# Optimization experiments

Measured on AMD Instinct MI355X. Metric: run time of the kernel, lower is better.

Reference implementation:

```python
import jax, jax.numpy as jnp
import numpy as np

B, S, HID = 2, 1024, 4096
N_HEADS, N_KV_HEADS = 32, 8
HEAD_DIM = HID // N_HEADS          # 128
N_REP = N_HEADS // N_KV_HEADS      # 4
ROPE_THETA = 10000.0


def setup_inputs() -> dict:
    key = jax.random.key(0)
    ks = jax.random.split(key, 5)
    scale = 0.02  # keep logits in a sane range
    return {
        "hidden_states": jax.random.normal(ks[0], (B, S, HID), dtype=jnp.float32),
        "Wq": jax.random.normal(ks[1], (HID, HID), dtype=jnp.float32) * scale,
        "Wk": jax.random.normal(ks[2], (N_KV_HEADS * HEAD_DIM, HID), dtype=jnp.float32) * scale,
        "Wv": jax.random.normal(ks[3], (N_KV_HEADS * HEAD_DIM, HID), dtype=jnp.float32) * scale,
        "Wo": jax.random.normal(ks[4], (HID, HID), dtype=jnp.float32) * scale,
    }


def _rope(x, cos, sin):
    # x: [B, H, S, D]; pairs are adjacent (view_as_complex on reshape(..., -1, 2))
    xe = x[..., 0::2]
    xo = x[..., 1::2]
    # cos/sin: [S, D/2] -> broadcast [1, 1, S, D/2]
    oe = xe * cos - xo * sin
    oo = xe * sin + xo * cos
    return jnp.stack([oe, oo], axis=-1).reshape(x.shape)


def reference(hidden_states, Wq, Wk, Wv, Wo):
    b, s, _ = hidden_states.shape
    q = (hidden_states @ Wq.T).reshape(b, s, N_HEADS, HEAD_DIM).transpose(0, 2, 1, 3)
    k = (hidden_states @ Wk.T).reshape(b, s, N_KV_HEADS, HEAD_DIM).transpose(0, 2, 1, 3)
    v = (hidden_states @ Wv.T).reshape(b, s, N_KV_HEADS, HEAD_DIM).transpose(0, 2, 1, 3)

    # RoPE (prefill: positions = arange(s))
    pos = jnp.arange(s, dtype=jnp.float32)
    inv_freq = 1.0 / (ROPE_THETA ** (jnp.arange(0, HEAD_DIM, 2, dtype=jnp.float32) / HEAD_DIM))
    freqs = pos[:, None] * inv_freq[None, :]  # [S, D/2]
    cos, sin = jnp.cos(freqs), jnp.sin(freqs)
    q = _rope(q, cos, sin)
    k = _rope(k, cos, sin)

    # GQA: repeat kv heads (repeat_kv expands each kv head n_rep times contiguously)
    k = jnp.repeat(k, N_REP, axis=1)  # [B, nH, S, D]
    v = jnp.repeat(v, N_REP, axis=1)

    scores = jnp.einsum("bhsd,bhtd->bhst", q, k) / jnp.sqrt(jnp.float32(HEAD_DIM))
    causal = jnp.tril(jnp.ones((s, s), dtype=bool))  # [S, S]
    scores = jnp.where(causal[None, None], scores, jnp.finfo(scores.dtype).min)
    attn = jax.nn.softmax(scores, axis=-1)
    out = jnp.einsum("bhst,bhtd->bhsd", attn, v)  # [B, nH, S, D]
    out = out.transpose(0, 2, 1, 3).reshape(b, s, HID)
    return out @ Wo.T
```

## Files before the change

kernel.cpp:

```cpp
#include <hip/hip_runtime.h>

typedef unsigned int u32;
typedef unsigned short u16;

#define S_LEN 1024
#define NH 32
#define NKV 8
#define DW 64
#define NEG_BIG (-1e30f)

typedef __bf16 bf16x8 __attribute__((ext_vector_type(8)));
typedef float f32x4 __attribute__((ext_vector_type(4)));

__device__ __forceinline__ u16 f2bf(float f) {
  u32 u = __builtin_bit_cast(u32, f);
  u += 0x7fffu + ((u >> 16) & 1u);
  return (u16)(u >> 16);
}
__device__ __forceinline__ float bflo(u32 u) { return __builtin_bit_cast(float, u << 16); }
__device__ __forceinline__ float bfhi(u32 u) { return __builtin_bit_cast(float, u & 0xffff0000u); }

__device__ __forceinline__ void gl_lds16(const u16* g, u32* l) {
  __builtin_amdgcn_global_load_lds(
      (__attribute__((address_space(1))) void*)const_cast<u16*>(g),
      (__attribute__((address_space(3))) void*)l, 16, 0, 0);
}

__launch_bounds__(256)
__global__ void cvt_bf16(const float4* __restrict__ in, uint4* __restrict__ out, int n8) {
  int i = blockIdx.x * 256 + threadIdx.x;
  if (i >= n8) return;
  float4 a = in[2 * i], b = in[2 * i + 1];
  uint4 o;
  o.x = (u32)f2bf(a.x) | ((u32)f2bf(a.y) << 16);
  o.y = (u32)f2bf(a.z) | ((u32)f2bf(a.w) << 16);
  o.z = (u32)f2bf(b.x) | ((u32)f2bf(b.y) << 16);
  o.w = (u32)f2bf(b.z) | ((u32)f2bf(b.w) << 16);
  out[i] = o;
}

template <bool BF16OUT, bool SPLIT>
__launch_bounds__(256)
__global__ void gemm16(const u16* __restrict__ A, const u16* __restrict__ B,
                       void* __restrict__ Cv, void* __restrict__ Cv2,
                       int M, int N, int K) {
  __shared__ u32 As[128 * 16];
  __shared__ u32 Bs[128 * 16];
  const int tid = threadIdx.x;
  const int lane = tid & 63, w = tid >> 6;
  const int wr = w >> 1, wc = w & 1;
  const int col = lane & 15, quad = lane >> 4;
  const int nwg = gridDim.x * gridDim.y;
  const int bid = blockIdx.y * gridDim.x + blockIdx.x;
  const int cpx = nwg >> 3;
  const int sw = (bid & 7) * cpx + (bid >> 3);
  const int m0 = (sw / gridDim.x) * 128, n0 = (sw % gridDim.x) * 128;

  const u16* ap0 = A + (size_t)(m0 + (tid >> 2)) * K + (tid & 3) * 8;
  const u16* ap1 = ap0 + (size_t)64 * K;
  const u16* bp0 = B + (size_t)(n0 + (tid >> 2)) * K + (tid & 3) * 8;
  const u16* bp1 = bp0 + (size_t)64 * K;
  u32* asd0 = &As[w * 256];
  u32* asd1 = &As[1024 + w * 256];
  u32* bsd0 = &Bs[w * 256];
  u32* bsd1 = &Bs[1024 + w * 256];

  f32x4 acc[4][4] = {};

  for (int k0 = 0; k0 < K; k0 += 32) {
    gl_lds16(ap0 + k0, asd0);
    gl_lds16(ap1 + k0, asd1);
    gl_lds16(bp0 + k0, bsd0);
    gl_lds16(bp1 + k0, bsd1);
    __syncthreads();

    bf16x8 af[4], bfr[4];
#pragma unroll
    for (int i = 0; i < 4; ++i) {
      int m = wr * 64 + i * 16 + col;
      af[i] = *reinterpret_cast<const bf16x8*>(&As[m * 16 + quad * 4]);
      int n = wc * 64 + i * 16 + col;
      bfr[i] = *reinterpret_cast<const bf16x8*>(&Bs[n * 16 + quad * 4]);
    }
#pragma unroll
    for (int i = 0; i < 4; ++i)
#pragma unroll
      for (int j = 0; j < 4; ++j)
        acc[i][j] = __builtin_amdgcn_mfma_f32_16x16x32_bf16(af[i], bfr[j], acc[i][j], 0, 0, 0);
    __syncthreads();
  }

#pragma unroll
  for (int i = 0; i < 4; ++i)
#pragma unroll
    for (int j = 0; j < 4; ++j)
#pragma unroll
      for (int r = 0; r < 4; ++r) {
        int row = m0 + wr * 64 + i * 16 + quad * 4 + r;
        int cc  = n0 + wc * 64 + j * 16 + col;
        float v = acc[i][j][r];
        if constexpr (SPLIT) {
          u16* dst = (cc >> 10) ? (u16*)Cv2 : (u16*)Cv;
          dst[(size_t)row * 1024 + (cc & 1023)] = f2bf(v);
        } else if constexpr (BF16OUT) {
          ((u16*)Cv)[(size_t)row * N + cc] = f2bf(v);
        } else {
          ((float*)Cv)[(size_t)row * N + cc] = v;
        }
      }
}

__launch_bounds__(256)
__global__ void rope_kernel(u32* __restrict__ buf, int heads, int npairs, float out_scale) {
  int p = blockIdx.x * 256 + threadIdx.x;
  if (p >= npairs) return;
  int d2 = p & 63;
  int s = (p / (64 * heads)) % S_LEN;
  float ang = (float)s * expf((float)d2 * -0.14391156831212787f);
  float sn, cs;
  sincosf(ang, &sn, &cs);
  u32 u = buf[p];
  float x0 = bflo(u), x1 = bfhi(u);
  float y0 = (x0 * cs - x1 * sn) * out_scale;
  float y1 = (x0 * sn + x1 * cs) * out_scale;
  buf[p] = (u32)f2bf(y0) | ((u32)f2bf(y1) << 16);
}

__launch_bounds__(256)
__global__ void attn_kernel(const u32* __restrict__ Qb, const u32* __restrict__ Kb,
                            const u32* __restrict__ Vb, u32* __restrict__ Ob) {
  __shared__ u32 Ks[64 * 64];
  __shared__ u32 Vt[128 * 32];
  __shared__ u16 Ps[4][16 * 64];
  const int tid = threadIdx.x, lane = tid & 63, w = tid >> 6;
  const int col = lane & 15, quad = lane >> 4;
  const int id = blockIdx.x;
  const int kh = id & 7;
  const int j2 = id >> 3;
  const int b = j2 & 1, hin = (j2 >> 1) & 3, pair = j2 >> 3;
  const int h = kh * 4 + hin;

  uint4 kpf[4], vpa[2], vpb[2];
  auto prefetch = [&](int t0) {
#pragma unroll
    for (int i = 0; i < 4; ++i) {
      int f = i * 256 + tid;
      int row = f >> 4, c4 = f & 15;
      kpf[i] = *((const uint4*)(Kb + ((size_t)((b * S_LEN + t0 + row) * NKV + kh)) * DW) + c4);
    }
#pragma unroll
    for (int i = 0; i < 2; ++i) {
      int f = i * 256 + tid;
      int kp = f & 31, c8 = f >> 5;
      size_t base0 = ((size_t)((b * S_LEN + t0 + 2 * kp) * NKV + kh)) * DW;
      vpa[i] = *((const uint4*)(Vb + base0) + c8);
      vpb[i] = *((const uint4*)(Vb + base0 + (size_t)NKV * DW) + c8);
    }
  };

  prefetch(0);

  for (int half = 0; half < 2; ++half) {
    const int jt = half ? pair : (15 - pair);
    const int q0 = jt * 64 + w * 16;

    bf16x8 qf[4];
    {
      const u32* qrow = Qb + ((size_t)((b * S_LEN + q0 + col) * NH + h)) * DW;
#pragma unroll
      for (int dc = 0; dc < 4; ++dc)
        qf[dc] = *reinterpret_cast<const bf16x8*>(qrow + dc * 16 + quad * 4);
    }

    float m_r[4], l_r[4];
    f32x4 oacc[8];
#pragma unroll
    for (int r = 0; r < 4; ++r) { m_r[r] = NEG_BIG; l_r[r] = 0.f; }
#pragma unroll
    for (int dt = 0; dt < 8; ++dt) oacc[dt] = (f32x4){0.f, 0.f, 0.f, 0.f};

    for (int tt = 0; tt <= jt; ++tt) {
      const int t0 = tt * 64;
      __syncthreads();
#pragma unroll
      for (int i = 0; i < 4; ++i) {
        int f = i * 256 + tid;
        int row = f >> 4, c4 = f & 15;
        *(uint4*)&Ks[(row * 64 + c4 * 4) ^ ((row & 7) << 2)] = kpf[i];
      }
#pragma unroll
      for (int i = 0; i < 2; ++i) {
        int f = i * 256 + tid;
        int kp = f & 31, c8 = f >> 5;
        u32 a[4] = {vpa[i].x, vpa[i].y, vpa[i].z, vpa[i].w};
        u32 bbv[4] = {vpb[i].x, vpb[i].y, vpb[i].z, vpb[i].w};
#pragma unroll
        for (int t = 0; t < 4; ++t) {
          int d0 = c8 * 8 + 2 * t, d1 = d0 + 1;
          u32 lo = (a[t] & 0xffffu) | (bbv[t] << 16);
          u32 hi = (a[t] >> 16) | (bbv[t] & 0xffff0000u);
          Vt[(d0 * 32 + kp) ^ ((d0 & 7) << 2)] = lo;
          Vt[(d1 * 32 + kp) ^ ((d1 & 7) << 2)] = hi;
        }
      }
      __syncthreads();

      if (tt < jt) prefetch(t0 + 64);
      else if (half == 0) prefetch(0);

      f32x4 sacc[4];
#pragma unroll
      for (int kt = 0; kt < 4; ++kt) sacc[kt] = (f32x4){0.f, 0.f, 0.f, 0.f};
      __builtin_amdgcn_s_setprio(1);
#pragma unroll
      for (int dc = 0; dc < 4; ++dc)
#pragma unroll
        for (int kt = 0; kt < 4; ++kt) {
          int key = kt * 16 + col;
          bf16x8 kf = *reinterpret_cast<const bf16x8*>(
              &Ks[(key * 64 + dc * 16 + quad * 4) ^ ((key & 7) << 2)]);
          sacc[kt] = __builtin_amdgcn_mfma_f32_16x16x32_bf16(qf[dc], kf, sacc[kt], 0, 0, 0);
        }
      __builtin_amdgcn_s_setprio(0);

      if (tt == jt) {
#pragma unroll
        for (int kt = 0; kt < 4; ++kt)
#pragma unroll
          for (int r = 0; r < 4; ++r) {
            int tg = t0 + kt * 16 + col;
            int qg = q0 + quad * 4 + r;
            if (tg > qg) sacc[kt][r] = NEG_BIG;
          }
      }

      float mt[4];
#pragma unroll
      for (int r = 0; r < 4; ++r)
        mt[r] = fmaxf(fmaxf(sacc[0][r], sacc[1][r]), fmaxf(sacc[2][r], sacc[3][r]));
#pragma unroll
      for (int off = 1; off < 16; off <<= 1)
#pragma unroll
        for (int r = 0; r < 4; ++r) mt[r] = fmaxf(mt[r], __shfl_xor(mt[r], off));
      float alpha[4], ps[4];
#pragma unroll
      for (int r = 0; r < 4; ++r) {
        float mn = fmaxf(m_r[r], mt[r]);
        alpha[r] = __expf(m_r[r] - mn);
        m_r[r] = mn;
        ps[r] = 0.f;
      }
#pragma unroll
      for (int kt = 0; kt < 4; ++kt)
#pragma unroll
        for (int r = 0; r < 4; ++r) {
          float p = __expf(sacc[kt][r] - m_r[r]);
          u16 pb = f2bf(p);
          int rw = quad * 4 + r;
          Ps[w][(rw * 64 + kt * 16 + col) ^ ((rw & 7) << 3)] = pb;
          ps[r] += bflo((u32)pb);
        }
#pragma unroll
      for (int off = 1; off < 16; off <<= 1)
#pragma unroll
        for (int r = 0; r < 4; ++r) ps[r] += __shfl_xor(ps[r], off);
#pragma unroll
      for (int r = 0; r < 4; ++r) l_r[r] = l_r[r] * alpha[r] + ps[r];
#pragma unroll
      for (int dt = 0; dt < 8; ++dt)
#pragma unroll
        for (int r = 0; r < 4; ++r) oacc[dt][r] *= alpha[r];

      bf16x8 pa[2];
#pragma unroll
      for (int ks = 0; ks < 2; ++ks)
        pa[ks] = *reinterpret_cast<const bf16x8*>(
            &Ps[w][(col * 64 + ks * 32 + quad * 8) ^ ((col & 7) << 3)]);
      __builtin_amdgcn_s_setprio(1);
#pragma unroll
      for (int dt = 0; dt < 8; ++dt) {
        int d = dt * 16 + col;
#pragma unroll
        for (int ks = 0; ks < 2; ++ks) {
          bf16x8 vf = *reinterpret_cast<const bf16x8*>(
              &Vt[(d * 32 + ks * 16 + quad * 4) ^ ((d & 7) << 2)]);
          oacc[dt] = __builtin_amdgcn_mfma_f32_16x16x32_bf16(pa[ks], vf, oacc[dt], 0, 0, 0);
        }
      }
      __builtin_amdgcn_s_setprio(0);
    }

    float invl[4];
#pragma unroll
    for (int r = 0; r < 4; ++r) invl[r] = 1.0f / l_r[r];
    u16* O16 = (u16*)Ob;
#pragma unroll
    for (int dt = 0; dt < 8; ++dt)
#pragma unroll
      for (int r = 0; r < 4; ++r) {
        int qg = q0 + quad * 4 + r;
        int d = dt * 16 + col;
        O16[((size_t)((b * S_LEN + qg) * NH + h)) * 128 + d] = f2bf(oacc[dt][r] * invl[r]);
      }
  }
}

extern "C" void kernel_launch(void* const* d_in, const int* in_sizes, int n_in,
                              void* d_out, int out_size, void* d_ws, size_t ws_size,
                              hipStream_t stream) {
  const float* hs = (const float*)d_in[0];
  const float* Wq = (const float*)d_in[1];
  const float* Wk = (const float*)d_in[2];
  const float* Wv = (const float*)d_in[3];
  const float* Wo = (const float*)d_in[4];

  u16* Qb   = (u16*)d_out;
  u16* hs16 = (u16*)((char*)d_out + (16u << 20));
  char* ws = (char*)d_ws;
  u16* Kb  = (u16*)ws;
  u16* Vb  = (u16*)(ws + (4u << 20));
  u16* Ob  = (u16*)(ws + (8u << 20));
  u16* Wsc = (u16*)(ws + (24u << 20));

  dim3 blk(256);
  cvt_bf16<<<4096, blk, 0, stream>>>((const float4*)hs, (uint4*)hs16, 1048576);
  cvt_bf16<<<8192, blk, 0, stream>>>((const float4*)Wq, (uint4*)Wsc, 2097152);
  gemm16<true, false><<<dim3(32, 16), blk, 0, stream>>>(hs16, Wsc, (void*)Qb, nullptr,
                                                        2048, 4096, 4096);
  cvt_bf16<<<2048, blk, 0, stream>>>((const float4*)Wk, (uint4*)Wsc, 524288);
  cvt_bf16<<<2048, blk, 0, stream>>>((const float4*)Wv, (uint4*)(Wsc + 1024 * 4096), 524288);
  gemm16<true, true><<<dim3(16, 16), blk, 0, stream>>>(hs16, Wsc, (void*)Kb, (void*)Vb,
                                                       2048, 2048, 4096);
  rope_kernel<<<16384, blk, 0, stream>>>((u32*)Qb, NH, 2048 * NH * 64, 0.08838834764831845f);
  rope_kernel<<<4096, blk, 0, stream>>>((u32*)Kb, NKV, 2048 * NKV * 64, 1.0f);
  cvt_bf16<<<8192, blk, 0, stream>>>((const float4*)Wo, (uint4*)Wsc, 2097152);
  attn_kernel<<<dim3(512), blk, 0, stream>>>((const u32*)Qb, (const u32*)Kb,
                                             (const u32*)Vb, (u32*)Ob);
  gemm16<false, false><<<dim3(32, 16), blk, 0, stream>>>(Ob, Wsc, d_out, nullptr,
                                                         2048, 4096, 4096);
}
```

Baseline: 621.0 us.

## Fuse Q/K/V projections into one GEMM and merge conversion and RoPE launches

Concatenates the bf16 Wq, Wk and Wv into one 6144-row weight so a single GEMM (48x16 tiles) computes Q, K and V, routing output columns to three buffers. The weight and activation conversions become one launch, as do the two RoPE passes. The tile-to-XCD mapping is changed so each XCD handles a contiguous 8-row by N/4-column block, aiming at better L2 reuse. This cuts launch count and fills the GPU better than the separate 512- and 256-tile GEMMs, at the cost of more index arithmetic and reuse of the workspace region shared by Wqkv and Ob.

```diff
diff --git a/kernel.cpp b/kernel.cpp
--- a/kernel.cpp
+++ b/kernel.cpp
@@ -24,6 +24,27 @@
   __builtin_amdgcn_global_load_lds(
       (__attribute__((address_space(1))) void*)const_cast<u16*>(g),
       (__attribute__((address_space(3))) void*)l, 16, 0, 0);
+}
+
+__launch_bounds__(256)
+__global__ void cvt_all(const float4* __restrict__ hs, const float4* __restrict__ wq,
+                        const float4* __restrict__ wk, const float4* __restrict__ wv,
+                        uint4* __restrict__ hs16, uint4* __restrict__ wqkv) {
+  const int b = blockIdx.x;
+  const float4* src;
+  uint4* dst;
+  int i;
+  if (b < 4096)       { i = b * 256 + threadIdx.x;           src = hs; dst = hs16; }
+  else if (b < 12288) { i = (b - 4096) * 256 + threadIdx.x;  src = wq; dst = wqkv; }
+  else if (b < 14336) { i = (b - 12288) * 256 + threadIdx.x; src = wk; dst = wqkv + 2097152; }
+  else                { i = (b - 14336) * 256 + threadIdx.x; src = wv; dst = wqkv + 2621440; }
+  float4 a = src[2 * i], c = src[2 * i + 1];
+  uint4 o;
+  o.x = (u32)f2bf(a.x) | ((u32)f2bf(a.y) << 16);
+  o.y = (u32)f2bf(a.z) | ((u32)f2bf(a.w) << 16);
+  o.z = (u32)f2bf(c.x) | ((u32)f2bf(c.y) << 16);
+  o.w = (u32)f2bf(c.z) | ((u32)f2bf(c.w) << 16);
+  dst[i] = o;
 }
 
 __launch_bounds__(256)
@@ -39,11 +60,11 @@
   out[i] = o;
 }
 
-template <bool BF16OUT, bool SPLIT>
+template <int MODE>
 __launch_bounds__(256)
 __global__ void gemm16(const u16* __restrict__ A, const u16* __restrict__ B,
-                       void* __restrict__ Cv, void* __restrict__ Cv2,
-                       int M, int N, int K) {
+                       void* __restrict__ C0, void* __restrict__ C1,
+                       void* __restrict__ C2, int M, int N, int K) {
   __shared__ u32 As[128 * 16];
   __shared__ u32 Bs[128 * 16];
   const int tid = threadIdx.x;
@@ -53,8 +74,12 @@
   const int nwg = gridDim.x * gridDim.y;
   const int bid = blockIdx.y * gridDim.x + blockIdx.x;
   const int cpx = nwg >> 3;
-  const int sw = (bid & 7) * cpx + (bid >> 3);
-  const int m0 = (sw / gridDim.x) * 128, n0 = (sw % gridDim.x) * 128;
+  const int chn = cpx >> 3;
+  const int xcd = bid & 7, q = bid >> 3;
+  const int cm = xcd >> 2, cn = xcd & 3;
+  const int im = q / chn, in_ = q % chn;
+  const int m0 = (cm * 8 + im) * 128;
+  const int n0 = (cn * chn + in_) * 128;
 
   const u16* ap0 = A + (size_t)(m0 + (tid >> 2)) * K + (tid & 3) * 8;
   const u16* ap1 = ap0 + (size_t)64 * K;
@@ -99,21 +124,24 @@
         int row = m0 + wr * 64 + i * 16 + quad * 4 + r;
         int cc  = n0 + wc * 64 + j * 16 + col;
         float v = acc[i][j][r];
-        if constexpr (SPLIT) {
-          u16* dst = (cc >> 10) ? (u16*)Cv2 : (u16*)Cv;
-          dst[(size_t)row * 1024 + (cc & 1023)] = f2bf(v);
-        } else if constexpr (BF16OUT) {
-          ((u16*)Cv)[(size_t)row * N + cc] = f2bf(v);
+        if constexpr (MODE == 2) {
+          if (cc < 4096)      ((u16*)C0)[(size_t)row * 4096 + cc] = f2bf(v);
+          else if (cc < 5120) ((u16*)C1)[(size_t)row * 1024 + (cc - 4096)] = f2bf(v);
+          else                ((u16*)C2)[(size_t)row * 1024 + (cc - 5120)] = f2bf(v);
         } else {
-          ((float*)Cv)[(size_t)row * N + cc] = v;
-        }
-      }
-}
-
-__launch_bounds__(256)
-__global__ void rope_kernel(u32* __restrict__ buf, int heads, int npairs, float out_scale) {
-  int p = blockIdx.x * 256 + threadIdx.x;
-  if (p >= npairs) return;
+          ((float*)C0)[(size_t)row * N + cc] = v;
+        }
+      }
+}
+
+__launch_bounds__(256)
+__global__ void rope_all(u32* __restrict__ Qb, u32* __restrict__ Kb) {
+  int pg = blockIdx.x * 256 + threadIdx.x;
+  u32* buf;
+  int p, heads;
+  float scale;
+  if (pg < 4194304) { buf = Qb; p = pg; heads = NH; scale = 0.08838834764831845f; }
+  else              { buf = Kb; p = pg - 4194304; heads = NKV; scale = 1.0f; }
   int d2 = p & 63;
   int s = (p / (64 * heads)) % S_LEN;
   float ang = (float)s * expf((float)d2 * -0.14391156831212787f);
@@ -121,8 +149,8 @@
   sincosf(ang, &sn, &cs);
   u32 u = buf[p];
   float x0 = bflo(u), x1 = bfhi(u);
-  float y0 = (x0 * cs - x1 * sn) * out_scale;
-  float y1 = (x0 * sn + x1 * cs) * out_scale;
+  float y0 = (x0 * cs - x1 * sn) * scale;
+  float y1 = (x0 * sn + x1 * cs) * scale;
   buf[p] = (u32)f2bf(y0) | ((u32)f2bf(y1) << 16);
 }
 
@@ -317,25 +345,22 @@
   u16* Qb   = (u16*)d_out;
   u16* hs16 = (u16*)((char*)d_out + (16u << 20));
   char* ws = (char*)d_ws;
-  u16* Kb  = (u16*)ws;
-  u16* Vb  = (u16*)(ws + (4u << 20));
-  u16* Ob  = (u16*)(ws + (8u << 20));
-  u16* Wsc = (u16*)(ws + (24u << 20));
+  u16* Kb   = (u16*)ws;
+  u16* Vb   = (u16*)(ws + (4u << 20));
+  u16* Wqkv = (u16*)(ws + (8u << 20));
+  u16* Ob   = (u16*)(ws + (8u << 20));
+  u16* Wo16 = (u16*)(ws + (24u << 20));
 
   dim3 blk(256);
-  cvt_bf16<<<4096, blk, 0, stream>>>((const float4*)hs, (uint4*)hs16, 1048576);
-  cvt_bf16<<<8192, blk, 0, stream>>>((const float4*)Wq, (uint4*)Wsc, 2097152);
-  gemm16<true, false><<<dim3(32, 16), blk, 0, stream>>>(hs16, Wsc, (void*)Qb, nullptr,
-                                                        2048, 4096, 4096);
-  cvt_bf16<<<2048, blk, 0, stream>>>((const float4*)Wk, (uint4*)Wsc, 524288);
-  cvt_bf16<<<2048, blk, 0, stream>>>((const float4*)Wv, (uint4*)(Wsc + 1024 * 4096), 524288);
-  gemm16<true, true><<<dim3(16, 16), blk, 0, stream>>>(hs16, Wsc, (void*)Kb, (void*)Vb,
-                                                       2048, 2048, 4096);
-  rope_kernel<<<16384, blk, 0, stream>>>((u32*)Qb, NH, 2048 * NH * 64, 0.08838834764831845f);
-  rope_kernel<<<4096, blk, 0, stream>>>((u32*)Kb, NKV, 2048 * NKV * 64, 1.0f);
-  cvt_bf16<<<8192, blk, 0, stream>>>((const float4*)Wo, (uint4*)Wsc, 2097152);
+  cvt_all<<<16384, blk, 0, stream>>>((const float4*)hs, (const float4*)Wq,
+                                     (const float4*)Wk, (const float4*)Wv,
+                                     (uint4*)hs16, (uint4*)Wqkv);
+  gemm16<2><<<dim3(48, 16), blk, 0, stream>>>(hs16, Wqkv, (void*)Qb, (void*)Kb,
+                                              (void*)Vb, 2048, 6144, 4096);
+  rope_all<<<20480, blk, 0, stream>>>((u32*)Qb, (u32*)Kb);
+  cvt_bf16<<<8192, blk, 0, stream>>>((const float4*)Wo, (uint4*)Wo16, 2097152);
   attn_kernel<<<dim3(512), blk, 0, stream>>>((const u32*)Qb, (const u32*)Kb,
                                              (const u32*)Vb, (u32*)Ob);
-  gemm16<false, false><<<dim3(32, 16), blk, 0, stream>>>(Ob, Wsc, d_out, nullptr,
-                                                         2048, 4096, 4096);
-}
+  gemm16<0><<<dim3(32, 16), blk, 0, stream>>>(Ob, Wo16, d_out, nullptr, nullptr,
+                                              2048, 4096, 4096);
+}
```

Result: faster. 547.1 us (-11.9%).
